# Optimization experiments

Hardware: AMD Instinct MI355X
Metric: run time of the kernel (lower is better)

Reference implementation:

```python
import jax, jax.numpy as jnp
import numpy as np

NEG_SLOPE = 0.2
STRONG_CONVEXITY = 0.5


def _scalar(x, Wq, Wl, bl, Wz, wz_out, wq_out, wl_out):
    # x: [B, D]; Wq/Wl: [L, H, D]; bl: [L, H]; Wz: [L-1, H, H]
    # Precompute all per-layer x-dependent terms in two batched einsums.
    qx = jnp.einsum('lhd,bd->lbh', Wq, x) ** 2          # [L, B, H]
    lx = jnp.einsum('lhd,bd->lbh', Wl, x) + bl[:, None, :]  # [L, B, H]
    z = jax.nn.leaky_relu(qx[0] + lx[0], negative_slope=NEG_SLOPE)

    def step(z, inputs):
        W, q, l = inputs
        z = jax.nn.leaky_relu(z @ W.T + q + l, negative_slope=NEG_SLOPE)
        return z, None

    z, _ = jax.lax.scan(step, z, (Wz, qx[1:], lx[1:]))
    # Final layer to scalar output (no bias on last wx_lin per torch code).
    out = z @ wz_out.T + (x @ wq_out.T) ** 2 + x @ wl_out.T  # [B, 1]
    return out


def setup_inputs() -> dict:
    key = jax.random.key(0)
    ks = jax.random.split(key, 8)
    B, D, H, L = 8192, 128, 512, 10
    f32 = jnp.float32
    x = jax.random.normal(ks[0], (B, D), f32)
    Wq = jax.random.normal(ks[1], (L, H, D), f32) * (1.0 / np.sqrt(D))
    Wl = jax.random.normal(ks[2], (L, H, D), f32) * (1.0 / np.sqrt(D))
    bl = jax.random.normal(ks[3], (L, H), f32) * 0.01
    # wz weights are kept non-negative in the original (clamp/exp init)
    Wz = jnp.abs(jax.random.normal(ks[4], (L - 1, H, H), f32)) * (1.0 / np.sqrt(H))
    wz_out = jnp.abs(jax.random.normal(ks[5], (1, H), f32)) * (1.0 / np.sqrt(H))
    wq_out = jax.random.normal(ks[6], (1, D), f32) * (1.0 / np.sqrt(D))
    wl_out = jax.random.normal(ks[7], (1, D), f32) * (1.0 / np.sqrt(D))
    return {"x": x, "Wq": Wq, "Wl": Wl, "bl": bl, "Wz": Wz,
            "wz_out": wz_out, "wq_out": wq_out, "wl_out": wl_out}


def reference(x, Wq, Wl, bl, Wz, wz_out, wq_out, wl_out):
    # forward = (1 - mu) * d(scalar)/dx + mu * x, with grad_outputs = ones
    def scalar_sum(xx):
        return jnp.sum(_scalar(xx, Wq, Wl, bl, Wz, wz_out, wq_out, wl_out))

    gx = jax.grad(scalar_sum)(x)  # per-sample gradient, [B, D]
    return (1.0 - STRONG_CONVEXITY) * gx + STRONG_CONVEXITY * x
```

## Files before the change

### kernel.cpp

```cpp
#include <hip/hip_runtime.h>


#define Bn 8192
#define Dn 128
#define Hn 512
#define Ln 10

constexpr float NS = 0.2f;

typedef __attribute__((ext_vector_type(8))) short short8;
typedef __attribute__((ext_vector_type(4))) float f32x4;

typedef const __attribute__((address_space(1))) void GV;
typedef __attribute__((address_space(3))) void LV;

__device__ __forceinline__ void gload16(const void* g, void* l) {
    __builtin_amdgcn_global_load_lds((GV*)g, (LV*)l, 16, 0, 0);
}

#define MFMA(acc, a, b) acc = __builtin_amdgcn_mfma_f32_16x16x32_bf16(a, b, acc, 0, 0, 0)

__device__ __forceinline__ unsigned short bf16_rne(float v) {
    unsigned u = __float_as_uint(v);
    u += 0x7FFFu + ((u >> 16) & 1u);
    return (unsigned short)(u >> 16);
}
__device__ __forceinline__ float bf2f(unsigned short h) {
    return __uint_as_float(((unsigned)h) << 16);
}
__device__ __forceinline__ void split2(float v, unsigned short& h, unsigned short& l) {
    h = bf16_rne(v);
    l = bf16_rne(v - bf2f(h));
}


__global__ __launch_bounds__(256) void split_flat(const float* __restrict__ in,
        unsigned short* __restrict__ hi, unsigned short* __restrict__ lo, int n4) {
    int i = blockIdx.x * 256 + threadIdx.x;
    if (i >= n4) return;
    float4 v = ((const float4*)in)[i];
    ushort4 h, l;
    split2(v.x, h.x, l.x);
    split2(v.y, h.y, l.y);
    split2(v.z, h.z, l.z);
    split2(v.w, h.w, l.w);
    ((ushort4*)hi)[i] = h;
    ((ushort4*)lo)[i] = l;
}

__global__ __launch_bounds__(256) void split_both(const float* __restrict__ in,
        unsigned short* __restrict__ hi, unsigned short* __restrict__ lo,
        unsigned short* __restrict__ thi, unsigned short* __restrict__ tlo,
        int R, int C) {
    __shared__ float t[32][33];
    const size_t off = (size_t)blockIdx.z * R * C;
    const float* src = in + off;
    unsigned short* sh_ = hi + off;
    unsigned short* sl_ = lo + off;
    unsigned short* dh = thi + off;
    unsigned short* dl = tlo + off;
    const int r0 = blockIdx.x * 32, c0 = blockIdx.y * 32;
    const int tr = threadIdx.x >> 5, tc = threadIdx.x & 31;
#pragma unroll
    for (int i = 0; i < 4; ++i) {
        size_t si = (size_t)(r0 + tr + 8 * i) * C + c0 + tc;
        float v = src[si];
        t[tr + 8 * i][tc] = v;
        unsigned short h, l; split2(v, h, l);
        sh_[si] = h; sl_[si] = l;
    }
    __syncthreads();
#pragma unroll
    for (int i = 0; i < 4; ++i) {
        float v = t[tc][tr + 8 * i];
        unsigned short h, l; split2(v, h, l);
        size_t o = (size_t)(c0 + tr + 8 * i) * R + r0 + tc;
        dh[o] = h; dl[o] = l;
    }
}


__global__ __launch_bounds__(256) void fwd_mfma(
    const unsigned short* __restrict__ xh, const unsigned short* __restrict__ xl,
    const unsigned short* __restrict__ zph, const unsigned short* __restrict__ zpl,
    const unsigned short* __restrict__ Wzh, const unsigned short* __restrict__ Wzl,
    const unsigned short* __restrict__ Wqh, const unsigned short* __restrict__ Wql,
    const unsigned short* __restrict__ Wlh, const unsigned short* __restrict__ Wll,
    const float* __restrict__ bl,
    unsigned short* __restrict__ zoh, unsigned short* __restrict__ zol,
    unsigned short* __restrict__ mask16,
    unsigned short* __restrict__ uoh, unsigned short* __restrict__ uol, int hasZ)
{
    __shared__ __align__(16) char smem[32768];
    unsigned short* Ah  = (unsigned short*)smem;
    unsigned short* Al  = (unsigned short*)(smem + 8192);
    unsigned short* B0h = (unsigned short*)(smem + 16384);
    unsigned short* B0l = (unsigned short*)(smem + 20480);
    unsigned short* B1h = (unsigned short*)(smem + 24576);
    unsigned short* B1l = (unsigned short*)(smem + 28672);

    const int tid = threadIdx.x;
    const int w = tid >> 6, lane = tid & 63;
    const int lq = lane >> 4, lc = lane & 15;
    const int wm = (w & 1) * 64, wn = (w >> 1) * 32;
    const int xcd = blockIdx.x & 7, slot = blockIdx.x >> 3;
    const int row0 = (xcd * 8 + (slot >> 3)) * 128, col0 = (slot & 7) * 64;
    const int sr = lane >> 2, sk = (lane & 3) * 8;

    f32x4 accz[4][2], accu[4][2], accv[4][2];
#pragma unroll
    for (int i = 0; i < 4; ++i)
#pragma unroll
        for (int j = 0; j < 2; ++j)
#pragma unroll
            for (int r = 0; r < 4; ++r) { accz[i][j][r] = 0.f; accu[i][j][r] = 0.f; accv[i][j][r] = 0.f; }

    if (hasZ) {
        for (int k0 = 0; k0 < Hn; k0 += 32) {
            __syncthreads();
            for (int c = w; c < 8; c += 4) {
                size_t go = (size_t)(row0 + c * 16 + sr) * Hn + k0 + sk;
                gload16(zph + go, Ah + c * 512);
                gload16(zpl + go, Al + c * 512);
            }
            {
                int c = w;
                size_t go = (size_t)(col0 + c * 16 + sr) * Hn + k0 + sk;
                gload16(Wzh + go, B0h + c * 512);
                gload16(Wzl + go, B0l + c * 512);
            }
            __syncthreads();
            short8 ah[4], al[4];
#pragma unroll
            for (int mt = 0; mt < 4; ++mt) {
                int ao = (wm + mt * 16 + lc) * 32 + lq * 8;
                ah[mt] = *(const short8*)(Ah + ao);
                al[mt] = *(const short8*)(Al + ao);
            }
#pragma unroll
            for (int nt = 0; nt < 2; ++nt) {
                int bo = (wn + nt * 16 + lc) * 32 + lq * 8;
                short8 bh = *(const short8*)(B0h + bo);
                short8 bv = *(const short8*)(B0l + bo);
#pragma unroll
                for (int mt = 0; mt < 4; ++mt) {
                    MFMA(accz[mt][nt], ah[mt], bh);
                    MFMA(accz[mt][nt], ah[mt], bv);
                    MFMA(accz[mt][nt], al[mt], bh);
                }
            }
        }
    }

    for (int k0 = 0; k0 < Dn; k0 += 32) {
        __syncthreads();
        for (int c = w; c < 8; c += 4) {
            size_t go = (size_t)(row0 + c * 16 + sr) * Dn + k0 + sk;
            gload16(xh + go, Ah + c * 512);
            gload16(xl + go, Al + c * 512);
        }
        {
            int c = w;
            size_t go = (size_t)(col0 + c * 16 + sr) * Dn + k0 + sk;
            gload16(Wqh + go, B0h + c * 512);
            gload16(Wql + go, B0l + c * 512);
            gload16(Wlh + go, B1h + c * 512);
            gload16(Wll + go, B1l + c * 512);
        }
        __syncthreads();
        short8 ah[4], al[4];
#pragma unroll
        for (int mt = 0; mt < 4; ++mt) {
            int ao = (wm + mt * 16 + lc) * 32 + lq * 8;
            ah[mt] = *(const short8*)(Ah + ao);
            al[mt] = *(const short8*)(Al + ao);
        }
#pragma unroll
        for (int nt = 0; nt < 2; ++nt) {
            int bo = (wn + nt * 16 + lc) * 32 + lq * 8;
            short8 bqh = *(const short8*)(B0h + bo);
            short8 bql = *(const short8*)(B0l + bo);
            short8 blh = *(const short8*)(B1h + bo);
            short8 bll = *(const short8*)(B1l + bo);
#pragma unroll
            for (int mt = 0; mt < 4; ++mt) {
                MFMA(accu[mt][nt], ah[mt], bqh);
                MFMA(accu[mt][nt], ah[mt], bql);
                MFMA(accu[mt][nt], al[mt], bqh);
                MFMA(accv[mt][nt], ah[mt], blh);
                MFMA(accv[mt][nt], ah[mt], bll);
                MFMA(accv[mt][nt], al[mt], blh);
            }
        }
    }

#pragma unroll
    for (int nt = 0; nt < 2; ++nt) {
        const int colb = col0 + wn + nt * 16;
        const int col = colb + lc;
        const float blv = bl[col];
#pragma unroll
        for (int mt = 0; mt < 4; ++mt) {
            const int rowb = row0 + wm + mt * 16;
#pragma unroll
            for (int r = 0; r < 4; ++r) {
                float uq = accu[mt][nt][r];
                float pre = accz[mt][nt][r] + uq * uq + accv[mt][nt][r] + blv;
                bool m = pre >= 0.f;
                unsigned long long bal = __ballot(m);
                if (lc == 0) {
                    int rw = rowb + lq * 4 + r;
                    mask16[(size_t)rw * 32 + (colb >> 4)] =
                        (unsigned short)((bal >> (lq * 16)) & 0xFFFFull);
                }
                float zv = m ? pre : NS * pre;
                unsigned short h, l; split2(zv, h, l);
                size_t o = (size_t)(rowb + lq * 4 + r) * Hn + col;
                zoh[o] = h; zol[o] = l;
                unsigned short uhh, ull; split2(uq, uhh, ull);
                uoh[o] = uhh; uol[o] = ull;
            }
        }
    }
}


__global__ __launch_bounds__(256) void bwd_combo(
    const unsigned short* __restrict__ gah, const unsigned short* __restrict__ gal,
    const unsigned short* __restrict__ WzTh, const unsigned short* __restrict__ WzTl,
    const unsigned short* __restrict__ maskprev,
    unsigned short* __restrict__ goh, unsigned short* __restrict__ gol,
    const unsigned short* __restrict__ uh_, const unsigned short* __restrict__ ul_,
    const unsigned short* __restrict__ WqTh, const unsigned short* __restrict__ WqTl,
    const unsigned short* __restrict__ WlTh, const unsigned short* __restrict__ WlTl,
    float* __restrict__ gx, int addTo, int nG, int finalF,
    const float* __restrict__ xin, const float* __restrict__ s,
    const float* __restrict__ wq_out, const float* __restrict__ wl_out)
{
    __shared__ __align__(16) char smem[16384];
    unsigned short* Ah = (unsigned short*)smem;
    unsigned short* Al = (unsigned short*)(smem + 4096);
    unsigned short* Bh = (unsigned short*)(smem + 8192);
    unsigned short* Bl = (unsigned short*)(smem + 12288);

    const int bid = blockIdx.x;
    const int tid = threadIdx.x;
    const int w = tid >> 6, lane = tid & 63;
    const int lq = lane >> 4, lc = lane & 15;
    const int sr = lane >> 2, sk = (lane & 3) * 8;
    const int wm = (w & 1) * 32, wn = (w >> 1) * 32;

    f32x4 acc[2][2];
#pragma unroll
    for (int i = 0; i < 2; ++i)
#pragma unroll
        for (int j = 0; j < 2; ++j)
#pragma unroll
            for (int r = 0; r < 4; ++r) acc[i][j][r] = 0.f;

    if (bid < nG) {
        const int xcd = bid & 7, slot = bid >> 3;
        const int row0 = (xcd * 16 + (slot >> 3)) * 64, col0 = (slot & 7) * 64;

        for (int k0 = 0; k0 < Hn; k0 += 32) {
            __syncthreads();
            {
                size_t ga_ = (size_t)(row0 + w * 16 + sr) * Hn + k0 + sk;
                gload16(gah + ga_, Ah + w * 512);
                gload16(gal + ga_, Al + w * 512);
                size_t gb_ = (size_t)(col0 + w * 16 + sr) * Hn + k0 + sk;
                gload16(WzTh + gb_, Bh + w * 512);
                gload16(WzTl + gb_, Bl + w * 512);
            }
            __syncthreads();
            short8 ah[2], al[2];
#pragma unroll
            for (int mt = 0; mt < 2; ++mt) {
                int ao = (wm + mt * 16 + lc) * 32 + lq * 8;
                ah[mt] = *(const short8*)(Ah + ao);
                al[mt] = *(const short8*)(Al + ao);
            }
#pragma unroll
            for (int nt = 0; nt < 2; ++nt) {
                int bo = (wn + nt * 16 + lc) * 32 + lq * 8;
                short8 bh = *(const short8*)(Bh + bo);
                short8 bv = *(const short8*)(Bl + bo);
#pragma unroll
                for (int mt = 0; mt < 2; ++mt) {
                    MFMA(acc[mt][nt], ah[mt], bh);
                    MFMA(acc[mt][nt], ah[mt], bv);
                    MFMA(acc[mt][nt], al[mt], bh);
                }
            }
        }

#pragma unroll
        for (int nt = 0; nt < 2; ++nt) {
            const int colb = col0 + wn + nt * 16;
            const int col = colb + lc;
#pragma unroll
            for (int mt = 0; mt < 2; ++mt) {
                const int rowb = row0 + wm + mt * 16;
#pragma unroll
                for (int r = 0; r < 4; ++r) {
                    int row = rowb + lq * 4 + r;
                    unsigned short wbits = maskprev[(size_t)row * 32 + (colb >> 4)];
                    float f = ((wbits >> lc) & 1) ? 1.f : NS;
                    float v = acc[mt][nt][r] * f;
                    unsigned short h, l; split2(v, h, l);
                    size_t o = (size_t)row * Hn + col;
                    goh[o] = h; gol[o] = l;
                }
            }
        }
    } else {
        const int t = bid - nG;
        const int xcd = t & 7, slot = t >> 3;
        const int row0 = (xcd * 16 + (slot >> 1)) * 64, col0 = (slot & 1) * 64;

        for (int j = 0; j < 32; ++j) {
            const int pass = j >> 4, k0 = (j & 15) * 32;
            __syncthreads();
            if (pass == 0) {
                size_t ga_ = (size_t)(row0 + w * 16 + sr) * Hn + k0 + sk;
                ushort4 gh0 = *(const ushort4*)(gah + ga_);
                ushort4 gh1 = *(const ushort4*)(gah + ga_ + 4);
                ushort4 gl0 = *(const ushort4*)(gal + ga_);
                ushort4 gl1 = *(const ushort4*)(gal + ga_ + 4);
                ushort4 vh0 = *(const ushort4*)(uh_ + ga_);
                ushort4 vh1 = *(const ushort4*)(uh_ + ga_ + 4);
                ushort4 vl0 = *(const ushort4*)(ul_ + ga_);
                ushort4 vl1 = *(const ushort4*)(ul_ + ga_ + 4);
                ushort4 oh0, oh1, ol0, ol1;
                float g, u, a;
                g = bf2f(gh0.x) + bf2f(gl0.x); u = bf2f(vh0.x) + bf2f(vl0.x);
                a = 2.f * u * g; split2(a, oh0.x, ol0.x);
                g = bf2f(gh0.y) + bf2f(gl0.y); u = bf2f(vh0.y) + bf2f(vl0.y);
                a = 2.f * u * g; split2(a, oh0.y, ol0.y);
                g = bf2f(gh0.z) + bf2f(gl0.z); u = bf2f(vh0.z) + bf2f(vl0.z);
                a = 2.f * u * g; split2(a, oh0.z, ol0.z);
                g = bf2f(gh0.w) + bf2f(gl0.w); u = bf2f(vh0.w) + bf2f(vl0.w);
                a = 2.f * u * g; split2(a, oh0.w, ol0.w);
                g = bf2f(gh1.x) + bf2f(gl1.x); u = bf2f(vh1.x) + bf2f(vl1.x);
                a = 2.f * u * g; split2(a, oh1.x, ol1.x);
                g = bf2f(gh1.y) + bf2f(gl1.y); u = bf2f(vh1.y) + bf2f(vl1.y);
                a = 2.f * u * g; split2(a, oh1.y, ol1.y);
                g = bf2f(gh1.z) + bf2f(gl1.z); u = bf2f(vh1.z) + bf2f(vl1.z);
                a = 2.f * u * g; split2(a, oh1.z, ol1.z);
                g = bf2f(gh1.w) + bf2f(gl1.w); u = bf2f(vh1.w) + bf2f(vl1.w);
                a = 2.f * u * g; split2(a, oh1.w, ol1.w);
                int lo_ = (w * 16 + sr) * 32 + sk;
                *(ushort4*)(Ah + lo_) = oh0; *(ushort4*)(Ah + lo_ + 4) = oh1;
                *(ushort4*)(Al + lo_) = ol0; *(ushort4*)(Al + lo_ + 4) = ol1;
                size_t gb_ = (size_t)(col0 + w * 16 + sr) * Hn + k0 + sk;
                gload16(WqTh + gb_, Bh + w * 512);
                gload16(WqTl + gb_, Bl + w * 512);
            } else {
                size_t ga_ = (size_t)(row0 + w * 16 + sr) * Hn + k0 + sk;
                gload16(gah + ga_, Ah + w * 512);
                gload16(gal + ga_, Al + w * 512);
                size_t gb_ = (size_t)(col0 + w * 16 + sr) * Hn + k0 + sk;
                gload16(WlTh + gb_, Bh + w * 512);
                gload16(WlTl + gb_, Bl + w * 512);
            }
            __syncthreads();
            short8 ah[2], al[2];
#pragma unroll
            for (int mt = 0; mt < 2; ++mt) {
                int ao = (wm + mt * 16 + lc) * 32 + lq * 8;
                ah[mt] = *(const short8*)(Ah + ao);
                al[mt] = *(const short8*)(Al + ao);
            }
#pragma unroll
            for (int nt = 0; nt < 2; ++nt) {
                int bo = (wn + nt * 16 + lc) * 32 + lq * 8;
                short8 bh = *(const short8*)(Bh + bo);
                short8 bv = *(const short8*)(Bl + bo);
#pragma unroll
                for (int mt = 0; mt < 2; ++mt) {
                    MFMA(acc[mt][nt], ah[mt], bh);
                    MFMA(acc[mt][nt], ah[mt], bv);
                    MFMA(acc[mt][nt], al[mt], bh);
                }
            }
        }

#pragma unroll
        for (int nt = 0; nt < 2; ++nt) {
            const int col = col0 + wn + nt * 16 + lc;
#pragma unroll
            for (int mt = 0; mt < 2; ++mt) {
                const int rowb = row0 + wm + mt * 16;
#pragma unroll
                for (int r = 0; r < 4; ++r) {
                    const int row = rowb + lq * 4 + r;
                    size_t o = (size_t)row * Dn + col;
                    float v = acc[mt][nt][r];
                    if (addTo) v += gx[o];
                    if (finalF) {
                        v = 0.5f * v + s[row] * wq_out[col] + 0.5f * wl_out[col]
                            + 0.5f * xin[o];
                    }
                    gx[o] = v;
                }
            }
        }
    }
}


__global__ __launch_bounds__(256) void ga_init(
    const float* __restrict__ wz_out, const unsigned short* __restrict__ mask9,
    unsigned short* __restrict__ gh, unsigned short* __restrict__ gl)
{
    int i = blockIdx.x * 256 + threadIdx.x;
    int e = i << 2;
    int b = e >> 9, h = e & 511;
    unsigned short wbits = mask9[(size_t)b * 32 + (h >> 4)];
    float4 wv = *(const float4*)(wz_out + h);
    int sh = h & 15;
    ushort4 oh, ol;
    float f;
    f = wv.x * (((wbits >> (sh + 0)) & 1) ? 1.f : NS); split2(f, oh.x, ol.x);
    f = wv.y * (((wbits >> (sh + 1)) & 1) ? 1.f : NS); split2(f, oh.y, ol.y);
    f = wv.z * (((wbits >> (sh + 2)) & 1) ? 1.f : NS); split2(f, oh.z, ol.z);
    f = wv.w * (((wbits >> (sh + 3)) & 1) ? 1.f : NS); split2(f, oh.w, ol.w);
    *(ushort4*)(gh + e) = oh;
    *(ushort4*)(gl + e) = ol;
}

__global__ __launch_bounds__(256) void rowdot_kernel(
    const float* __restrict__ x, const float* __restrict__ wq_out, float* __restrict__ s) {
    const int b = blockIdx.x * 4 + (threadIdx.x >> 6);
    const int lane = threadIdx.x & 63;
    float v = x[(size_t)b * Dn + lane] * wq_out[lane] +
              x[(size_t)b * Dn + 64 + lane] * wq_out[64 + lane];
#pragma unroll
    for (int off = 32; off > 0; off >>= 1) v += __shfl_down(v, off, 64);
    if (lane == 0) s[b] = v;
}


extern "C" void kernel_launch(void* const* d_in, const int* in_sizes, int n_in,
                              void* d_out, int out_size, void* d_ws, size_t ws_size,
                              hipStream_t stream) {
    (void)in_sizes; (void)n_in; (void)out_size; (void)ws_size;
    const float* x      = (const float*)d_in[0];
    const float* Wq     = (const float*)d_in[1];
    const float* Wl     = (const float*)d_in[2];
    const float* bl     = (const float*)d_in[3];
    const float* Wz     = (const float*)d_in[4];
    const float* wz_out = (const float*)d_in[5];
    const float* wq_out = (const float*)d_in[6];
    const float* wl_out = (const float*)d_in[7];
    float* out = (float*)d_out;

    char* p = (char*)d_ws;
    #define CARVE(name, bytes) unsigned short* name = (unsigned short*)p; p += (((size_t)(bytes)) + 255) & ~(size_t)255;
    CARVE(xh,  (size_t)Bn*Dn*2)  CARVE(xl,  (size_t)Bn*Dn*2)
    CARVE(Wqh, (size_t)Ln*Hn*Dn*2) CARVE(Wql, (size_t)Ln*Hn*Dn*2)
    CARVE(Wlh, (size_t)Ln*Hn*Dn*2) CARVE(Wll, (size_t)Ln*Hn*Dn*2)
    CARVE(WqTh,(size_t)Ln*Hn*Dn*2) CARVE(WqTl,(size_t)Ln*Hn*Dn*2)
    CARVE(WlTh,(size_t)Ln*Hn*Dn*2) CARVE(WlTl,(size_t)Ln*Hn*Dn*2)
    CARVE(Wzh, (size_t)(Ln-1)*Hn*Hn*2) CARVE(Wzl, (size_t)(Ln-1)*Hn*Hn*2)
    CARVE(WzTh,(size_t)(Ln-1)*Hn*Hn*2) CARVE(WzTl,(size_t)(Ln-1)*Hn*Hn*2)
    CARVE(zAh, (size_t)Bn*Hn*2) CARVE(zAl, (size_t)Bn*Hn*2)
    CARVE(zBh, (size_t)Bn*Hn*2) CARVE(zBl, (size_t)Bn*Hn*2)
    CARVE(uLh, (size_t)Ln*Bn*Hn*2) CARVE(uLl, (size_t)Ln*Bn*Hn*2)
    float* s = (float*)p; p += (size_t)Bn*4;
    unsigned short* mask16 = (unsigned short*)p; p += (size_t)Ln*Bn*32*2;
    #undef CARVE

    split_flat<<<(Bn*Dn/4 + 255)/256, 256, 0, stream>>>(x, xh, xl, Bn*Dn/4);
    split_both<<<dim3(Hn/32, Dn/32, Ln), 256, 0, stream>>>(Wq, Wqh, Wql, WqTh, WqTl, Hn, Dn);
    split_both<<<dim3(Hn/32, Dn/32, Ln), 256, 0, stream>>>(Wl, Wlh, Wll, WlTh, WlTl, Hn, Dn);
    split_both<<<dim3(Hn/32, Hn/32, Ln-1), 256, 0, stream>>>(Wz, Wzh, Wzl, WzTh, WzTl, Hn, Hn);

    rowdot_kernel<<<Bn/4, 256, 0, stream>>>(x, wq_out, s);

    fwd_mfma<<<512, 256, 0, stream>>>(xh, xl, nullptr, nullptr, nullptr, nullptr,
        Wqh, Wql, Wlh, Wll, bl, zAh, zAl, mask16, uLh, uLl, 0);
    for (int l = 1; l < Ln; ++l) {
        const unsigned short* zh  = (l & 1) ? zAh : zBh;
        const unsigned short* zl_ = (l & 1) ? zAl : zBl;
        unsigned short* oh  = (l & 1) ? zBh : zAh;
        unsigned short* ol_ = (l & 1) ? zBl : zAl;
        fwd_mfma<<<512, 256, 0, stream>>>(xh, xl, zh, zl_,
            Wzh + (size_t)(l-1)*Hn*Hn, Wzl + (size_t)(l-1)*Hn*Hn,
            Wqh + (size_t)l*Hn*Dn, Wql + (size_t)l*Hn*Dn,
            Wlh + (size_t)l*Hn*Dn, Wll + (size_t)l*Hn*Dn,
            bl + (size_t)l*Hn, oh, ol_, mask16 + (size_t)l*Bn*32,
            uLh + (size_t)l*Bn*Hn, uLl + (size_t)l*Bn*Hn, 1);
    }

    ga_init<<<(Bn*Hn/4)/256, 256, 0, stream>>>(wz_out, mask16 + (size_t)9*Bn*32, zAh, zAl);
    for (int l = Ln - 1; l >= 0; --l) {
        int sidx = (Ln - 1 - l) & 1;
        const unsigned short* gh_  = sidx ? zBh : zAh;
        const unsigned short* gl_  = sidx ? zBl : zAl;
        unsigned short* oh   = sidx ? zAh : zBh;
        unsigned short* ol_  = sidx ? zAl : zBl;
        const int nG = (l > 0) ? 1024 : 0;
        bwd_combo<<<nG + 256, 256, 0, stream>>>(
            gh_, gl_,
            (l > 0) ? WzTh + (size_t)(l-1)*Hn*Hn : nullptr,
            (l > 0) ? WzTl + (size_t)(l-1)*Hn*Hn : nullptr,
            (l > 0) ? mask16 + (size_t)(l-1)*Bn*32 : nullptr,
            (l > 0) ? oh : nullptr, (l > 0) ? ol_ : nullptr,
            uLh + (size_t)l*Bn*Hn, uLl + (size_t)l*Bn*Hn,
            WqTh + (size_t)l*Dn*Hn, WqTl + (size_t)l*Dn*Hn,
            WlTh + (size_t)l*Dn*Hn, WlTl + (size_t)l*Dn*Hn,
            out, (l == Ln - 1) ? 0 : 1, nG, (l == 0) ? 1 : 0,
            x, s, wq_out, wl_out);
    }
}
```

Measured before the change: 863.6 us.

## Fuse backward layer loop into one persistent kernel with grid barriers

The ga_init kernel and the ten per-layer backward launches are replaced by one persistent kernel of 768 blocks that syncs layers through an atomic-counter grid barrier. The gradient-through-Wz GEMM also moves from 64-row tiles over 1024 blocks to 128-row tiles over 512 blocks, which reuses weight tiles more per block. This removes launch gaps and per-launch ramp-up and tail effects. In exchange it needs all 768 blocks co-resident, adds spin-wait barrier cost, and has a timeout guard that could silently break the sync.

```diff
diff --git a/kernel.cpp b/kernel.cpp
--- a/kernel.cpp
+++ b/kernel.cpp
@@ -6,6 +6,8 @@
 #define Hn 512
 #define Ln 10
 
+#define BWD_GRID 768
+
 constexpr float NS = 0.2f;
 
 typedef __attribute__((ext_vector_type(8))) short short8;
@@ -31,6 +33,21 @@
 __device__ __forceinline__ void split2(float v, unsigned short& h, unsigned short& l) {
     h = bf16_rne(v);
     l = bf16_rne(v - bf2f(h));
+}
+
+__device__ __forceinline__ void grid_bar(unsigned* cnt, unsigned target) {
+    __threadfence();
+    __syncthreads();
+    if (threadIdx.x == 0) {
+        atomicAdd(cnt, 1u);
+        unsigned guard = 0;
+        while (atomicAdd(cnt, 0u) < target) {
+            __builtin_amdgcn_s_sleep(2);
+            if (++guard > (1u << 24)) break;
+        }
+    }
+    __syncthreads();
+    __threadfence();
 }
 
 
@@ -80,18 +97,16 @@
 }
 
 
-__global__ __launch_bounds__(256) void fwd_mfma(
-    const unsigned short* __restrict__ xh, const unsigned short* __restrict__ xl,
-    const unsigned short* __restrict__ zph, const unsigned short* __restrict__ zpl,
-    const unsigned short* __restrict__ Wzh, const unsigned short* __restrict__ Wzl,
-    const unsigned short* __restrict__ Wqh, const unsigned short* __restrict__ Wql,
-    const unsigned short* __restrict__ Wlh, const unsigned short* __restrict__ Wll,
-    const float* __restrict__ bl,
-    unsigned short* __restrict__ zoh, unsigned short* __restrict__ zol,
-    unsigned short* __restrict__ mask16,
-    unsigned short* __restrict__ uoh, unsigned short* __restrict__ uol, int hasZ)
+__device__ __forceinline__ void fwd_layer_body(int bid, char* smem,
+    const unsigned short* xh, const unsigned short* xl,
+    const unsigned short* zph, const unsigned short* zpl,
+    const unsigned short* Wzh, const unsigned short* Wzl,
+    const unsigned short* Wqh, const unsigned short* Wql,
+    const unsigned short* Wlh, const unsigned short* Wll,
+    const float* bl,
+    unsigned short* zoh, unsigned short* zol,
+    unsigned short* mask16, unsigned short* uoh, unsigned short* uol, int hasZ)
 {
-    __shared__ __align__(16) char smem[32768];
     unsigned short* Ah  = (unsigned short*)smem;
     unsigned short* Al  = (unsigned short*)(smem + 8192);
     unsigned short* B0h = (unsigned short*)(smem + 16384);
@@ -103,7 +118,7 @@
     const int w = tid >> 6, lane = tid & 63;
     const int lq = lane >> 4, lc = lane & 15;
     const int wm = (w & 1) * 64, wn = (w >> 1) * 32;
-    const int xcd = blockIdx.x & 7, slot = blockIdx.x >> 3;
+    const int xcd = bid & 7, slot = bid >> 3;
     const int row0 = (xcd * 8 + (slot >> 3)) * 128, col0 = (slot & 7) * 64;
     const int sr = lane >> 2, sk = (lane & 3) * 8;
 
@@ -225,30 +240,111 @@
 }
 
 
-__global__ __launch_bounds__(256) void bwd_combo(
-    const unsigned short* __restrict__ gah, const unsigned short* __restrict__ gal,
-    const unsigned short* __restrict__ WzTh, const unsigned short* __restrict__ WzTl,
-    const unsigned short* __restrict__ maskprev,
-    unsigned short* __restrict__ goh, unsigned short* __restrict__ gol,
-    const unsigned short* __restrict__ uh_, const unsigned short* __restrict__ ul_,
-    const unsigned short* __restrict__ WqTh, const unsigned short* __restrict__ WqTl,
-    const unsigned short* __restrict__ WlTh, const unsigned short* __restrict__ WlTl,
-    float* __restrict__ gx, int addTo, int nG, int finalF,
-    const float* __restrict__ xin, const float* __restrict__ s,
-    const float* __restrict__ wq_out, const float* __restrict__ wl_out)
+__device__ __forceinline__ void bwd_g128_body(int bid, char* smem,
+    const unsigned short* gah, const unsigned short* gal,
+    const unsigned short* WzTh, const unsigned short* WzTl,
+    const unsigned short* maskprev,
+    unsigned short* goh, unsigned short* gol)
 {
-    __shared__ __align__(16) char smem[16384];
+    unsigned short* Ah = (unsigned short*)smem;
+    unsigned short* Al = (unsigned short*)(smem + 8192);
+    unsigned short* Bh = (unsigned short*)(smem + 16384);
+    unsigned short* Bl = (unsigned short*)(smem + 20480);
+
+    const int tid = threadIdx.x;
+    const int w = tid >> 6, lane = tid & 63;
+    const int lq = lane >> 4, lc = lane & 15;
+    const int sr = lane >> 2, sk = (lane & 3) * 8;
+    const int wm = (w & 1) * 64, wn = (w >> 1) * 32;
+    const int xcd = bid & 7, slot = bid >> 3;
+    const int row0 = (xcd * 8 + (slot >> 3)) * 128, col0 = (slot & 7) * 64;
+
+    f32x4 acc[4][2];
+#pragma unroll
+    for (int i = 0; i < 4; ++i)
+#pragma unroll
+        for (int j = 0; j < 2; ++j)
+#pragma unroll
+            for (int r = 0; r < 4; ++r) acc[i][j][r] = 0.f;
+
+    for (int k0 = 0; k0 < Hn; k0 += 32) {
+        __syncthreads();
+        for (int cc = 0; cc < 2; ++cc) {
+            int c = w + cc * 4;
+            size_t ga_ = (size_t)(row0 + c * 16 + sr) * Hn + k0 + sk;
+            gload16(gah + ga_, Ah + c * 512);
+            gload16(gal + ga_, Al + c * 512);
+        }
+        {
+            int c = w;
+            size_t gb_ = (size_t)(col0 + c * 16 + sr) * Hn + k0 + sk;
+            gload16(WzTh + gb_, Bh + c * 512);
+            gload16(WzTl + gb_, Bl + c * 512);
+        }
+        __syncthreads();
+        short8 ah[4], al[4];
+#pragma unroll
+        for (int mt = 0; mt < 4; ++mt) {
+            int ao = (wm + mt * 16 + lc) * 32 + lq * 8;
+            ah[mt] = *(const short8*)(Ah + ao);
+            al[mt] = *(const short8*)(Al + ao);
+        }
+#pragma unroll
+        for (int nt = 0; nt < 2; ++nt) {
+            int bo = (wn + nt * 16 + lc) * 32 + lq * 8;
+            short8 bh = *(const short8*)(Bh + bo);
+            short8 bv = *(const short8*)(Bl + bo);
+#pragma unroll
+            for (int mt = 0; mt < 4; ++mt) {
+                MFMA(acc[mt][nt], ah[mt], bh);
+                MFMA(acc[mt][nt], ah[mt], bv);
+                MFMA(acc[mt][nt], al[mt], bh);
+            }
+        }
+    }
+
+#pragma unroll
+    for (int nt = 0; nt < 2; ++nt) {
+        const int colb = col0 + wn + nt * 16;
+        const int col = colb + lc;
+#pragma unroll
+        for (int mt = 0; mt < 4; ++mt) {
+            const int rowb = row0 + wm + mt * 16;
+#pragma unroll
+            for (int r = 0; r < 4; ++r) {
+                int row = rowb + lq * 4 + r;
+                unsigned short wbits = maskprev[(size_t)row * 32 + (colb >> 4)];
+                float f = ((wbits >> lc) & 1) ? 1.f : NS;
+                float v = acc[mt][nt][r] * f;
+                unsigned short h, l; split2(v, h, l);
+                size_t o = (size_t)row * Hn + col;
+                goh[o] = h; gol[o] = l;
+            }
+        }
+    }
+}
+
+__device__ __forceinline__ void bwd_x_body(int t, char* smem,
+    const unsigned short* gah, const unsigned short* gal,
+    const unsigned short* uh_, const unsigned short* ul_,
+    const unsigned short* WqTh, const unsigned short* WqTl,
+    const unsigned short* WlTh, const unsigned short* WlTl,
+    float* gx, int addTo, int finalF,
+    const float* xin, const float* s,
+    const float* wq_out, const float* wl_out)
+{
     unsigned short* Ah = (unsigned short*)smem;
     unsigned short* Al = (unsigned short*)(smem + 4096);
     unsigned short* Bh = (unsigned short*)(smem + 8192);
     unsigned short* Bl = (unsigned short*)(smem + 12288);
 
-    const int bid = blockIdx.x;
     const int tid = threadIdx.x;
     const int w = tid >> 6, lane = tid & 63;
     const int lq = lane >> 4, lc = lane & 15;
     const int sr = lane >> 2, sk = (lane & 3) * 8;
     const int wm = (w & 1) * 32, wn = (w >> 1) * 32;
+    const int xcd = t & 7, slot = t >> 3;
+    const int row0 = (xcd * 16 + (slot >> 1)) * 64, col0 = (slot & 1) * 64;
 
     f32x4 acc[2][2];
 #pragma unroll
@@ -258,162 +354,99 @@
 #pragma unroll
             for (int r = 0; r < 4; ++r) acc[i][j][r] = 0.f;
 
-    if (bid < nG) {
-        const int xcd = bid & 7, slot = bid >> 3;
-        const int row0 = (xcd * 16 + (slot >> 3)) * 64, col0 = (slot & 7) * 64;
-
-        for (int k0 = 0; k0 < Hn; k0 += 32) {
-            __syncthreads();
-            {
-                size_t ga_ = (size_t)(row0 + w * 16 + sr) * Hn + k0 + sk;
-                gload16(gah + ga_, Ah + w * 512);
-                gload16(gal + ga_, Al + w * 512);
-                size_t gb_ = (size_t)(col0 + w * 16 + sr) * Hn + k0 + sk;
-                gload16(WzTh + gb_, Bh + w * 512);
-                gload16(WzTl + gb_, Bl + w * 512);
-            }
-            __syncthreads();
-            short8 ah[2], al[2];
+    for (int j = 0; j < 32; ++j) {
+        const int pass = j >> 4, k0 = (j & 15) * 32;
+        __syncthreads();
+        if (pass == 0) {
+            size_t ga_ = (size_t)(row0 + w * 16 + sr) * Hn + k0 + sk;
+            ushort4 gh0 = *(const ushort4*)(gah + ga_);
+            ushort4 gh1 = *(const ushort4*)(gah + ga_ + 4);
+            ushort4 gl0 = *(const ushort4*)(gal + ga_);
+            ushort4 gl1 = *(const ushort4*)(gal + ga_ + 4);
+            ushort4 vh0 = *(const ushort4*)(uh_ + ga_);
+            ushort4 vh1 = *(const ushort4*)(uh_ + ga_ + 4);
+            ushort4 vl0 = *(const ushort4*)(ul_ + ga_);
+            ushort4 vl1 = *(const ushort4*)(ul_ + ga_ + 4);
+            ushort4 oh0, oh1, ol0, ol1;
+            float g, u, a;
+            g = bf2f(gh0.x) + bf2f(gl0.x); u = bf2f(vh0.x) + bf2f(vl0.x);
+            a = 2.f * u * g; split2(a, oh0.x, ol0.x);
+            g = bf2f(gh0.y) + bf2f(gl0.y); u = bf2f(vh0.y) + bf2f(vl0.y);
+            a = 2.f * u * g; split2(a, oh0.y, ol0.y);
+            g = bf2f(gh0.z) + bf2f(gl0.z); u = bf2f(vh0.z) + bf2f(vl0.z);
+            a = 2.f * u * g; split2(a, oh0.z, ol0.z);
+            g = bf2f(gh0.w) + bf2f(gl0.w); u = bf2f(vh0.w) + bf2f(vl0.w);
+            a = 2.f * u * g; split2(a, oh0.w, ol0.w);
+            g = bf2f(gh1.x) + bf2f(gl1.x); u = bf2f(vh1.x) + bf2f(vl1.x);
+            a = 2.f * u * g; split2(a, oh1.x, ol1.x);
+            g = bf2f(gh1.y) + bf2f(gl1.y); u = bf2f(vh1.y) + bf2f(vl1.y);
+            a = 2.f * u * g; split2(a, oh1.y, ol1.y);
+            g = bf2f(gh1.z) + bf2f(gl1.z); u = bf2f(vh1.z) + bf2f(vl1.z);
+            a = 2.f * u * g; split2(a, oh1.z, ol1.z);
+            g = bf2f(gh1.w) + bf2f(gl1.w); u = bf2f(vh1.w) + bf2f(vl1.w);
+            a = 2.f * u * g; split2(a, oh1.w, ol1.w);
+            int lo_ = (w * 16 + sr) * 32 + sk;
+            *(ushort4*)(Ah + lo_) = oh0; *(ushort4*)(Ah + lo_ + 4) = oh1;
+            *(ushort4*)(Al + lo_) = ol0; *(ushort4*)(Al + lo_ + 4) = ol1;
+            size_t gb_ = (size_t)(col0 + w * 16 + sr) * Hn + k0 + sk;
+            gload16(WqTh + gb_, Bh + w * 512);
+            gload16(WqTl + gb_, Bl + w * 512);
+        } else {
+            size_t ga_ = (size_t)(row0 + w * 16 + sr) * Hn + k0 + sk;
+            gload16(gah + ga_, Ah + w * 512);
+            gload16(gal + ga_, Al + w * 512);
+            size_t gb_ = (size_t)(col0 + w * 16 + sr) * Hn + k0 + sk;
+            gload16(WlTh + gb_, Bh + w * 512);
+            gload16(WlTl + gb_, Bl + w * 512);
+        }
+        __syncthreads();
+        short8 ah[2], al[2];
+#pragma unroll
+        for (int mt = 0; mt < 2; ++mt) {
+            int ao = (wm + mt * 16 + lc) * 32 + lq * 8;
+            ah[mt] = *(const short8*)(Ah + ao);
+            al[mt] = *(const short8*)(Al + ao);
+        }
+#pragma unroll
+        for (int nt = 0; nt < 2; ++nt) {
+            int bo = (wn + nt * 16 + lc) * 32 + lq * 8;
+            short8 bh = *(const short8*)(Bh + bo);
+            short8 bv = *(const short8*)(Bl + bo);
 #pragma unroll
             for (int mt = 0; mt < 2; ++mt) {
-                int ao = (wm + mt * 16 + lc) * 32 + lq * 8;
-                ah[mt] = *(const short8*)(Ah + ao);
-                al[mt] = *(const short8*)(Al + ao);
-            }
-#pragma unroll
-            for (int nt = 0; nt < 2; ++nt) {
-                int bo = (wn + nt * 16 + lc) * 32 + lq * 8;
-                short8 bh = *(const short8*)(Bh + bo);
-                short8 bv = *(const short8*)(Bl + bo);
-#pragma unroll
-                for (int mt = 0; mt < 2; ++mt) {
-                    MFMA(acc[mt][nt], ah[mt], bh);
-                    MFMA(acc[mt][nt], ah[mt], bv);
-                    MFMA(acc[mt][nt], al[mt], bh);
+                MFMA(acc[mt][nt], ah[mt], bh);
+                MFMA(acc[mt][nt], ah[mt], bv);
+                MFMA(acc[mt][nt], al[mt], bh);
+            }
+        }
+    }
+
+#pragma unroll
+    for (int nt = 0; nt < 2; ++nt) {
+        const int col = col0 + wn + nt * 16 + lc;
+#pragma unroll
+        for (int mt = 0; mt < 2; ++mt) {
+            const int rowb = row0 + wm + mt * 16;
+#pragma unroll
+            for (int r = 0; r < 4; ++r) {
+                const int row = rowb + lq * 4 + r;
+                size_t o = (size_t)row * Dn + col;
+                float v = acc[mt][nt][r];
+                if (addTo) v += gx[o];
+                if (finalF) {
+                    v = 0.5f * v + s[row] * wq_out[col] + 0.5f * wl_out[col]
+                        + 0.5f * xin[o];
                 }
-            }
-        }
-
-#pragma unroll
-        for (int nt = 0; nt < 2; ++nt) {
-            const int colb = col0 + wn + nt * 16;
-            const int col = colb + lc;
-#pragma unroll
-            for (int mt = 0; mt < 2; ++mt) {
-                const int rowb = row0 + wm + mt * 16;
-#pragma unroll
-                for (int r = 0; r < 4; ++r) {
-                    int row = rowb + lq * 4 + r;
-                    unsigned short wbits = maskprev[(size_t)row * 32 + (colb >> 4)];
-                    float f = ((wbits >> lc) & 1) ? 1.f : NS;
-                    float v = acc[mt][nt][r] * f;
-                    unsigned short h, l; split2(v, h, l);
-                    size_t o = (size_t)row * Hn + col;
-                    goh[o] = h; gol[o] = l;
-                }
-            }
-        }
-    } else {
-        const int t = bid - nG;
-        const int xcd = t & 7, slot = t >> 3;
-        const int row0 = (xcd * 16 + (slot >> 1)) * 64, col0 = (slot & 1) * 64;
-
-        for (int j = 0; j < 32; ++j) {
-            const int pass = j >> 4, k0 = (j & 15) * 32;
-            __syncthreads();
-            if (pass == 0) {
-                size_t ga_ = (size_t)(row0 + w * 16 + sr) * Hn + k0 + sk;
-                ushort4 gh0 = *(const ushort4*)(gah + ga_);
-                ushort4 gh1 = *(const ushort4*)(gah + ga_ + 4);
-                ushort4 gl0 = *(const ushort4*)(gal + ga_);
-                ushort4 gl1 = *(const ushort4*)(gal + ga_ + 4);
-                ushort4 vh0 = *(const ushort4*)(uh_ + ga_);
-                ushort4 vh1 = *(const ushort4*)(uh_ + ga_ + 4);
-                ushort4 vl0 = *(const ushort4*)(ul_ + ga_);
-                ushort4 vl1 = *(const ushort4*)(ul_ + ga_ + 4);
-                ushort4 oh0, oh1, ol0, ol1;
-                float g, u, a;
-                g = bf2f(gh0.x) + bf2f(gl0.x); u = bf2f(vh0.x) + bf2f(vl0.x);
-                a = 2.f * u * g; split2(a, oh0.x, ol0.x);
-                g = bf2f(gh0.y) + bf2f(gl0.y); u = bf2f(vh0.y) + bf2f(vl0.y);
-                a = 2.f * u * g; split2(a, oh0.y, ol0.y);
-                g = bf2f(gh0.z) + bf2f(gl0.z); u = bf2f(vh0.z) + bf2f(vl0.z);
-                a = 2.f * u * g; split2(a, oh0.z, ol0.z);
-                g = bf2f(gh0.w) + bf2f(gl0.w); u = bf2f(vh0.w) + bf2f(vl0.w);
-                a = 2.f * u * g; split2(a, oh0.w, ol0.w);
-                g = bf2f(gh1.x) + bf2f(gl1.x); u = bf2f(vh1.x) + bf2f(vl1.x);
-                a = 2.f * u * g; split2(a, oh1.x, ol1.x);
-                g = bf2f(gh1.y) + bf2f(gl1.y); u = bf2f(vh1.y) + bf2f(vl1.y);
-                a = 2.f * u * g; split2(a, oh1.y, ol1.y);
-                g = bf2f(gh1.z) + bf2f(gl1.z); u = bf2f(vh1.z) + bf2f(vl1.z);
-                a = 2.f * u * g; split2(a, oh1.z, ol1.z);
-                g = bf2f(gh1.w) + bf2f(gl1.w); u = bf2f(vh1.w) + bf2f(vl1.w);
-                a = 2.f * u * g; split2(a, oh1.w, ol1.w);
-                int lo_ = (w * 16 + sr) * 32 + sk;
-                *(ushort4*)(Ah + lo_) = oh0; *(ushort4*)(Ah + lo_ + 4) = oh1;
-                *(ushort4*)(Al + lo_) = ol0; *(ushort4*)(Al + lo_ + 4) = ol1;
-                size_t gb_ = (size_t)(col0 + w * 16 + sr) * Hn + k0 + sk;
-                gload16(WqTh + gb_, Bh + w * 512);
-                gload16(WqTl + gb_, Bl + w * 512);
-            } else {
-                size_t ga_ = (size_t)(row0 + w * 16 + sr) * Hn + k0 + sk;
-                gload16(gah + ga_, Ah + w * 512);
-                gload16(gal + ga_, Al + w * 512);
-                size_t gb_ = (size_t)(col0 + w * 16 + sr) * Hn + k0 + sk;
-                gload16(WlTh + gb_, Bh + w * 512);
-                gload16(WlTl + gb_, Bl + w * 512);
-            }
-            __syncthreads();
-            short8 ah[2], al[2];
-#pragma unroll
-            for (int mt = 0; mt < 2; ++mt) {
-                int ao = (wm + mt * 16 + lc) * 32 + lq * 8;
-                ah[mt] = *(const short8*)(Ah + ao);
-                al[mt] = *(const short8*)(Al + ao);
-            }
-#pragma unroll
-            for (int nt = 0; nt < 2; ++nt) {
-                int bo = (wn + nt * 16 + lc) * 32 + lq * 8;
-                short8 bh = *(const short8*)(Bh + bo);
-                short8 bv = *(const short8*)(Bl + bo);
-#pragma unroll
-                for (int mt = 0; mt < 2; ++mt) {
-                    MFMA(acc[mt][nt], ah[mt], bh);
-                    MFMA(acc[mt][nt], ah[mt], bv);
-                    MFMA(acc[mt][nt], al[mt], bh);
-                }
-            }
-        }
-
-#pragma unroll
-        for (int nt = 0; nt < 2; ++nt) {
-            const int col = col0 + wn + nt * 16 + lc;
-#pragma unroll
-            for (int mt = 0; mt < 2; ++mt) {
-                const int rowb = row0 + wm + mt * 16;
-#pragma unroll
-                for (int r = 0; r < 4; ++r) {
-                    const int row = rowb + lq * 4 + r;
-                    size_t o = (size_t)row * Dn + col;
-                    float v = acc[mt][nt][r];
-                    if (addTo) v += gx[o];
-                    if (finalF) {
-                        v = 0.5f * v + s[row] * wq_out[col] + 0.5f * wl_out[col]
-                            + 0.5f * xin[o];
-                    }
-                    gx[o] = v;
-                }
-            }
-        }
-    }
-}
-
-
-__global__ __launch_bounds__(256) void ga_init(
-    const float* __restrict__ wz_out, const unsigned short* __restrict__ mask9,
-    unsigned short* __restrict__ gh, unsigned short* __restrict__ gl)
+                gx[o] = v;
+            }
+        }
+    }
+}
+
+__device__ __forceinline__ void ga_init_elem(int i,
+    const float* wz_out, const unsigned short* mask9,
+    unsigned short* gh, unsigned short* gl)
 {
-    int i = blockIdx.x * 256 + threadIdx.x;
     int e = i << 2;
     int b = e >> 9, h = e & 511;
     unsigned short wbits = mask9[(size_t)b * 32 + (h >> 4)];
@@ -427,6 +460,64 @@
     f = wv.w * (((wbits >> (sh + 3)) & 1) ? 1.f : NS); split2(f, oh.w, ol.w);
     *(ushort4*)(gh + e) = oh;
     *(ushort4*)(gl + e) = ol;
+}
+
+
+__global__ __launch_bounds__(256) void fwd_mfma(
+    const unsigned short* xh, const unsigned short* xl,
+    const unsigned short* zph, const unsigned short* zpl,
+    const unsigned short* Wzh, const unsigned short* Wzl,
+    const unsigned short* Wqh, const unsigned short* Wql,
+    const unsigned short* Wlh, const unsigned short* Wll,
+    const float* bl, unsigned short* zoh, unsigned short* zol,
+    unsigned short* mask16, unsigned short* uoh, unsigned short* uol, int hasZ)
+{
+    __shared__ __align__(16) char smem[32768];
+    fwd_layer_body(blockIdx.x, smem, xh, xl, zph, zpl, Wzh, Wzl, Wqh, Wql,
+                   Wlh, Wll, bl, zoh, zol, mask16, uoh, uol, hasZ);
+}
+
+
+__global__ __launch_bounds__(256, 3) void bwd_fused(
+    const unsigned short* WzTh, const unsigned short* WzTl,
+    const unsigned short* WqTh, const unsigned short* WqTl,
+    const unsigned short* WlTh, const unsigned short* WlTl,
+    const unsigned short* uLh, const unsigned short* uLl,
+    const unsigned short* mask16,
+    unsigned short* zAh, unsigned short* zAl,
+    unsigned short* zBh, unsigned short* zBl,
+    const float* wz_out, const float* x, const float* s,
+    const float* wq_out, const float* wl_out,
+    float* out, unsigned* cnt)
+{
+    __shared__ __align__(16) char smem[24576];
+    for (int i = blockIdx.x * 256 + threadIdx.x; i < Bn * Hn / 4; i += BWD_GRID * 256)
+        ga_init_elem(i, wz_out, mask16 + (size_t)9 * Bn * 32, zAh, zAl);
+    unsigned phase = 1;
+    grid_bar(cnt, BWD_GRID * phase); ++phase;
+
+    for (int l = Ln - 1; l >= 0; --l) {
+        int sidx = (Ln - 1 - l) & 1;
+        const unsigned short* gh_ = sidx ? zBh : zAh;
+        const unsigned short* gl_ = sidx ? zBl : zAl;
+        unsigned short* oh = sidx ? zAh : zBh;
+        unsigned short* ol_ = sidx ? zAl : zBl;
+        if (blockIdx.x < 512) {
+            if (l > 0)
+                bwd_g128_body(blockIdx.x, smem, gh_, gl_,
+                    WzTh + (size_t)(l - 1) * Hn * Hn,
+                    WzTl + (size_t)(l - 1) * Hn * Hn,
+                    mask16 + (size_t)(l - 1) * Bn * 32, oh, ol_);
+        } else {
+            bwd_x_body(blockIdx.x - 512, smem, gh_, gl_,
+                uLh + (size_t)l * Bn * Hn, uLl + (size_t)l * Bn * Hn,
+                WqTh + (size_t)l * Dn * Hn, WqTl + (size_t)l * Dn * Hn,
+                WlTh + (size_t)l * Dn * Hn, WlTl + (size_t)l * Dn * Hn,
+                out, (l == Ln - 1) ? 0 : 1, (l == 0) ? 1 : 0,
+                x, s, wq_out, wl_out);
+        }
+        if (l > 0) { grid_bar(cnt, BWD_GRID * phase); ++phase; }
+    }
 }
 
 __global__ __launch_bounds__(256) void rowdot_kernel(
@@ -469,6 +560,7 @@
     CARVE(uLh, (size_t)Ln*Bn*Hn*2) CARVE(uLl, (size_t)Ln*Bn*Hn*2)
     float* s = (float*)p; p += (size_t)Bn*4;
     unsigned short* mask16 = (unsigned short*)p; p += (size_t)Ln*Bn*32*2;
+    unsigned* barCnt = (unsigned*)p; p += 256;
     #undef CARVE
 
     split_flat<<<(Bn*Dn/4 + 255)/256, 256, 0, stream>>>(x, xh, xl, Bn*Dn/4);
@@ -477,6 +569,7 @@
     split_both<<<dim3(Hn/32, Hn/32, Ln-1), 256, 0, stream>>>(Wz, Wzh, Wzl, WzTh, WzTl, Hn, Hn);
 
     rowdot_kernel<<<Bn/4, 256, 0, stream>>>(x, wq_out, s);
+    hipMemsetAsync(barCnt, 0, sizeof(unsigned), stream);
 
     fwd_mfma<<<512, 256, 0, stream>>>(xh, xl, nullptr, nullptr, nullptr, nullptr,
         Wqh, Wql, Wlh, Wll, bl, zAh, zAl, mask16, uLh, uLl, 0);
@@ -493,24 +586,7 @@
             uLh + (size_t)l*Bn*Hn, uLl + (size_t)l*Bn*Hn, 1);
     }
 
-    ga_init<<<(Bn*Hn/4)/256, 256, 0, stream>>>(wz_out, mask16 + (size_t)9*Bn*32, zAh, zAl);
-    for (int l = Ln - 1; l >= 0; --l) {
-        int sidx = (Ln - 1 - l) & 1;
-        const unsigned short* gh_  = sidx ? zBh : zAh;
-        const unsigned short* gl_  = sidx ? zBl : zAl;
-        unsigned short* oh   = sidx ? zAh : zBh;
-        unsigned short* ol_  = sidx ? zAl : zBl;
-        const int nG = (l > 0) ? 1024 : 0;
-        bwd_combo<<<nG + 256, 256, 0, stream>>>(
-            gh_, gl_,
-            (l > 0) ? WzTh + (size_t)(l-1)*Hn*Hn : nullptr,
-            (l > 0) ? WzTl + (size_t)(l-1)*Hn*Hn : nullptr,
-            (l > 0) ? mask16 + (size_t)(l-1)*Bn*32 : nullptr,
-            (l > 0) ? oh : nullptr, (l > 0) ? ol_ : nullptr,
-            uLh + (size_t)l*Bn*Hn, uLl + (size_t)l*Bn*Hn,
-            WqTh + (size_t)l*Dn*Hn, WqTl + (size_t)l*Dn*Hn,
-            WlTh + (size_t)l*Dn*Hn, WlTl + (size_t)l*Dn*Hn,
-            out, (l == Ln - 1) ? 0 : 1, nG, (l == 0) ? 1 : 0,
-            x, s, wq_out, wl_out);
-    }
-}
+    bwd_fused<<<BWD_GRID, 256, 0, stream>>>(
+        WzTh, WzTl, WqTh, WqTl, WlTh, WlTl, uLh, uLl, mask16,
+        zAh, zAl, zBh, zBl, wz_out, x, s, wq_out, wl_out, out, barCnt);
+}
```

Result: slower. 2.818 ms (+226.3%).
